# Kernel tuning notes

Hardware: AMD Instinct MI355X
Metric: run time of the kernel (lower is better)

Reference implementation:

```python
import jax, jax.numpy as jnp
import numpy as np

B, C, L, R, UNITS = 256, 32, 64, 64, 128


def setup_inputs() -> dict:
    key = jax.random.key(0)
    ks = jax.random.split(key, 6)
    D = C + 3 * UNITS  # input_dim = channels + 3*units

    def glorot(k, fan_in, fan_out):
        lim = float(np.sqrt(6.0 / (fan_in + fan_out)))
        return jax.random.uniform(k, (fan_in, fan_out), jnp.float32, -lim, lim)

    inputs = jax.random.normal(ks[0], (B, C, L, R), jnp.float32)
    wr = glorot(ks[1], D, 3 * UNITS)
    br = jnp.zeros((3 * UNITS,), jnp.float32)
    wz = glorot(ks[2], D, 4 * UNITS)
    bz = jnp.zeros((4 * UNITS,), jnp.float32)
    # orthogonal init approximated by scaled normal (math of forward unaffected)
    w_ij = jax.random.normal(ks[3], (C, UNITS), jnp.float32) / np.sqrt(C).astype(np.float32)
    b_ij = jnp.zeros((UNITS,), jnp.float32)
    U = jax.random.normal(ks[4], (3 * UNITS, UNITS), jnp.float32) / np.sqrt(3 * UNITS).astype(np.float32)
    return dict(inputs=inputs, wr=wr, br=br, wz=wz, bz=bz, w_ij=w_ij, b_ij=b_ij, U=U)


def _spatial_gru(inputs, wr, br, wz, bz, w_ij, b_ij, U):
    units = b_ij.shape[0]
    x = jnp.transpose(inputs, (2, 3, 0, 1))  # [L, R, B, C]  (direction 'lt')
    Ldim, Rdim, Bdim, _ = x.shape
    zeros = jnp.zeros((Bdim, units), x.dtype)

    def col_step(h_left, cell):
        h_top, h_diag, s_ij = cell  # each [B, units] / [B, C]
        # q = [h_top, h_left, h_diag, s_ij]  (matches torch cat order)
        q = jnp.concatenate([h_top, h_left, h_diag, s_ij], axis=1)
        r = jax.nn.sigmoid(q @ wr + br)                      # [B, 3U]
        z = (q @ wz + bz).reshape(Bdim, 4, units)
        zi, zl, zt, zd = jnp.moveaxis(jax.nn.softmax(z, axis=1), 1, 0)
        h_hat = jnp.tanh(
            s_ij @ w_ij + b_ij
            + (r * jnp.concatenate([h_left, h_top, h_diag], axis=1)) @ U
        )
        h = zl * h_left + zt * h_top + zd * h_diag + zi * h_hat
        return h, h

    def row_step(prev_row, x_row):
        # prev_row[j] is h_top for column j; prev_row[j-1] is h_diag (zero at j=0)
        diag_row = jnp.concatenate([zeros[None], prev_row[:-1]], axis=0)
        _, new_row = jax.lax.scan(col_step, zeros, (prev_row, diag_row, x_row))
        return new_row, None

    init_row = jnp.zeros((Rdim, Bdim, units), x.dtype)
    final_row, _ = jax.lax.scan(row_step, init_row, x)
    return final_row[-1]  # h at bottom-right cell, [B, units]


def reference(inputs, wr, br, wz, bz, w_ij, b_ij, U):
    return _spatial_gru(inputs, wr, br, wz, bz, w_ij, b_ij, U)
```

## Files before the change

### kernel.cpp

```cpp
#include <hip/hip_runtime.h>
#include <cstddef>

typedef _Float16 f16;
typedef unsigned int u32;
typedef __attribute__((ext_vector_type(8))) _Float16 half8;
typedef __attribute__((ext_vector_type(4))) _Float16 half4;
typedef __attribute__((ext_vector_type(4))) float f32x4;

#define BATCH 256
#define CH    32
#define LR    64
#define UNITS 128
#define DIN   416
#define NC    1024
#define KU    384

#define OFF_WH   0ull
#define OFF_WL   745472ull
#define OFF_W3H  1490944ull
#define OFF_W3L  1499136ull
#define OFF_BC   1507328ull
#define OFF_UH   1511424ull
#define OFF_UL   1609728ull
#define OFF_HHI  1708032ull
#define HPLANE   4194304ull
#define OFF_HLO  (OFF_HHI + 3ull*HPLANE)
#define OFF_G    (OFF_HLO + 3ull*HPLANE)

static __device__ __forceinline__ void gll16(const void* g, void* l) {
  __builtin_amdgcn_global_load_lds(
      (const __attribute__((address_space(1))) u32*)g,
      (__attribute__((address_space(3))) u32*)l, 16, 0, 0);
}
static __device__ __forceinline__ float fast_tanh(float x) {
  float e = __expf(-2.f * fabsf(x));
  float t = (1.f - e) / (1.f + e);
  return copysignf(t, x);
}

__global__ __launch_bounds__(256) void prep_kernel(
    const float* __restrict__ wr, const float* __restrict__ br,
    const float* __restrict__ wz, const float* __restrict__ bz,
    const float* __restrict__ w_ij, const float* __restrict__ b_ij,
    const float* __restrict__ U, char* __restrict__ ws) {
  int idx = blockIdx.x * 256 + threadIdx.x;
  if (idx < 896 * DIN) {
    int n = idx / DIN, k = idx % DIN;
    float v = (n < 384) ? wr[k * 384 + n] : wz[k * 512 + (n - 384)];
    f16 hi = (f16)v;
    ((f16*)(ws + OFF_WH))[idx] = hi;
    ((f16*)(ws + OFF_WL))[idx] = (f16)(v - (float)hi);
  }
  if (idx < 128 * 32) {
    int n3 = idx >> 5, k3 = idx & 31;
    float v = w_ij[k3 * UNITS + n3];
    f16 hi = (f16)v;
    ((f16*)(ws + OFF_W3H))[idx] = hi;
    ((f16*)(ws + OFF_W3L))[idx] = (f16)(v - (float)hi);
  }
  if (idx < UNITS * KU) {
    int n = idx / KU, k = idx % KU;
    float v = U[k * UNITS + n];
    f16 hi = (f16)v;
    ((f16*)(ws + OFF_UH))[idx] = hi;
    ((f16*)(ws + OFF_UL))[idx] = (f16)(v - (float)hi);
  }
  if (idx < NC) {
    float b;
    if (idx < 384)      b = br[idx];
    else if (idx < 896) b = bz[idx - 384];
    else                b = b_ij[idx - 896];
    ((float*)(ws + OFF_BC))[idx] = b;
  }
}

__global__ __launch_bounds__(256) void gemm_kernel(
    const float* __restrict__ inputs, char* __restrict__ ws, int d, int i0) {
  const int bx = blockIdx.x;
  const int cb = bx & 7, rb = (bx >> 3) & 1, ci = bx >> 4;
  const int i = i0 + ci, j = d - i;
  const int b0 = rb * 128, n0 = cb * 128;
  const int t = threadIdx.x;
  const int w = t >> 6, lane = t & 63;
  const int lm = lane & 15, ksl = lane >> 4;
  const int wrow = (w >> 1) * 64, wcol = (w & 1) * 64;

  __shared__ f16 Ah[4096], Al[4096], Bh[4096], Bl[4096];

  const int s0 = w * 128 + lane, s1 = s0 + 64;
  const int r0s = s0 >> 2, k0s = (s0 & 3) ^ ((r0s >> 1) & 3);
  const int r1s = s1 >> 2, k1s = (s1 & 3) ^ ((r1s >> 1) & 3);
  const u32 db0 = (u32)w * 2048u, db1 = db0 + 1024u;
  const int kswz = (ksl ^ ((lm >> 1) & 3)) * 8;

  const f16* __restrict__ H1h = (const f16*)(ws + OFF_HHI + (size_t)((d + 2) % 3) * HPLANE);
  const f16* __restrict__ H1l = (const f16*)(ws + OFF_HLO + (size_t)((d + 2) % 3) * HPLANE);
  const f16* __restrict__ H2h = (const f16*)(ws + OFF_HHI + (size_t)((d + 1) % 3) * HPLANE);
  const f16* __restrict__ H2l = (const f16*)(ws + OFF_HLO + (size_t)((d + 1) % 3) * HPLANE);
  const f16* __restrict__ Wh  = (const f16*)(ws + OFF_WH);
  const f16* __restrict__ Wl  = (const f16*)(ws + OFF_WL);
  const f16* __restrict__ W3h = (const f16*)(ws + OFF_W3H);
  const f16* __restrict__ W3l = (const f16*)(ws + OFF_W3L);
  const bool vt = (i > 0), vl = (j > 0), vd = (i > 0 && j > 0);

  f32x4 acc[4][4];
#pragma unroll
  for (int mi = 0; mi < 4; mi++)
#pragma unroll
    for (int ni = 0; ni < 4; ni++)
#pragma unroll
      for (int r = 0; r < 4; r++) acc[mi][ni][r] = 0.f;

  for (int kt = (cb == 7 ? 12 : 0); kt < 13; kt++) {
    const bool ok = (kt < 4) ? vt : (kt < 8) ? vl : (kt < 12) ? vd : true;
    if (!ok) continue;

    if (kt < 12) {
      const f16 *ph, *pl; int hrow;
      if (kt < 4)      { ph = H1h; pl = H1l; hrow = i - 1; }
      else if (kt < 8) { ph = H1h; pl = H1l; hrow = i; }
      else             { ph = H2h; pl = H2l; hrow = i - 1; }
      const size_t ab = ((size_t)hrow * BATCH + b0) * UNITS + (size_t)(kt & 3) * 32;
      gll16(ph + ab + r0s * UNITS + k0s * 8, (char*)Ah + db0);
      gll16(ph + ab + r1s * UNITS + k1s * 8, (char*)Ah + db1);
      gll16(pl + ab + r0s * UNITS + k0s * 8, (char*)Al + db0);
      gll16(pl + ab + r1s * UNITS + k1s * 8, (char*)Al + db1);
    } else {
      const int r = t >> 1, kp = (t & 1) * 2;
      const int b = b0 + r, sw = (r >> 1) & 3;
#pragma unroll
      for (int c2 = 0; c2 < 2; c2++) {
        const int c = kp + c2;
        half8 hv, lv;
#pragma unroll
        for (int q = 0; q < 8; q++) {
          float v = inputs[((size_t)b * CH + c * 8 + q) * (LR * LR) + i * LR + j];
          f16 h = (f16)v;
          hv[q] = h; lv[q] = (f16)(v - (float)h);
        }
        const int p = r * 4 + (c ^ sw);
        *(half8*)&Ah[p * 8] = hv;
        *(half8*)&Al[p * 8] = lv;
      }
    }
    if (cb < 7) {
      const size_t bb = (size_t)n0 * DIN + (size_t)kt * 32;
      gll16(Wh + bb + r0s * DIN + k0s * 8, (char*)Bh + db0);
      gll16(Wh + bb + r1s * DIN + k1s * 8, (char*)Bh + db1);
      gll16(Wl + bb + r0s * DIN + k0s * 8, (char*)Bl + db0);
      gll16(Wl + bb + r1s * DIN + k1s * 8, (char*)Bl + db1);
    } else {
      gll16(W3h + r0s * 32 + k0s * 8, (char*)Bh + db0);
      gll16(W3h + r1s * 32 + k1s * 8, (char*)Bh + db1);
      gll16(W3l + r0s * 32 + k0s * 8, (char*)Bl + db0);
      gll16(W3l + r1s * 32 + k1s * 8, (char*)Bl + db1);
    }
    __syncthreads();

    half8 afh[4], afl[4], bfh[4], bfl[4];
#pragma unroll
    for (int mi = 0; mi < 4; mi++) {
      const int ro = (wrow + mi * 16 + lm) * 32 + kswz;
      afh[mi] = *(const half8*)&Ah[ro];
      afl[mi] = *(const half8*)&Al[ro];
    }
#pragma unroll
    for (int ni = 0; ni < 4; ni++) {
      const int ro = (wcol + ni * 16 + lm) * 32 + kswz;
      bfh[ni] = *(const half8*)&Bh[ro];
      bfl[ni] = *(const half8*)&Bl[ro];
    }
#pragma unroll
    for (int mi = 0; mi < 4; mi++)
#pragma unroll
      for (int ni = 0; ni < 4; ni++) {
        acc[mi][ni] = __builtin_amdgcn_mfma_f32_16x16x32_f16(afh[mi], bfh[ni], acc[mi][ni], 0, 0, 0);
        acc[mi][ni] = __builtin_amdgcn_mfma_f32_16x16x32_f16(afl[mi], bfh[ni], acc[mi][ni], 0, 0, 0);
        acc[mi][ni] = __builtin_amdgcn_mfma_f32_16x16x32_f16(afh[mi], bfl[ni], acc[mi][ni], 0, 0, 0);
      }
    __syncthreads();
  }

  float* __restrict__ G = (float*)(ws + OFF_G) + (size_t)ci * BATCH * NC;
  const float* __restrict__ bc = (const float*)(ws + OFF_BC);
#pragma unroll
  for (int mi = 0; mi < 4; mi++)
#pragma unroll
    for (int ni = 0; ni < 4; ni++) {
      const int n = n0 + wcol + ni * 16 + lm;
      const float bb = bc[n];
#pragma unroll
      for (int r = 0; r < 4; r++) {
        const int b = b0 + wrow + mi * 16 + ksl * 4 + r;
        G[(size_t)b * NC + n] = acc[mi][ni][r] + bb;
      }
    }
}

__global__ __launch_bounds__(256) void gate_kernel(char* __restrict__ ws, int d, int i0) {
  const int bx = blockIdx.x;
  const int rb = bx & 7, ci = bx >> 3;
  const int i = i0 + ci, j = d - i;
  const int b0 = rb * 32;
  const int t = threadIdx.x;
  const int w = t >> 6, lane = t & 63;
  const int lm = lane & 15, ksl = lane >> 4;
  const int wcol = w * 32;

  __shared__ f16 Rh[32][40], Rl[32][40];
  __shared__ f16 Uh[4096], Ul[4096];

  const int s0 = w * 128 + lane, s1 = s0 + 64;
  const int r0s = s0 >> 2, k0s = (s0 & 3) ^ ((r0s >> 1) & 3);
  const int r1s = s1 >> 2, k1s = (s1 & 3) ^ ((r1s >> 1) & 3);
  const u32 db0 = (u32)w * 2048u, db1 = db0 + 1024u;
  const int kswz = (ksl ^ ((lm >> 1) & 3)) * 8;

  float* __restrict__ G = (float*)(ws + OFF_G) + (size_t)ci * BATCH * NC;
  const f16* __restrict__ H1h = (const f16*)(ws + OFF_HHI + (size_t)((d + 2) % 3) * HPLANE);
  const f16* __restrict__ H1l = (const f16*)(ws + OFF_HLO + (size_t)((d + 2) % 3) * HPLANE);
  const f16* __restrict__ H2h = (const f16*)(ws + OFF_HHI + (size_t)((d + 1) % 3) * HPLANE);
  const f16* __restrict__ H2l = (const f16*)(ws + OFF_HLO + (size_t)((d + 1) % 3) * HPLANE);
  f16* __restrict__ Hoh = (f16*)(ws + OFF_HHI + (size_t)(d % 3) * HPLANE);
  f16* __restrict__ Hol = (f16*)(ws + OFF_HLO + (size_t)(d % 3) * HPLANE);
  const f16* __restrict__ UhT = (const f16*)(ws + OFF_UH);
  const f16* __restrict__ UlT = (const f16*)(ws + OFF_UL);
  const bool vt = (i > 0), vlf = (j > 0), vd = (i > 0 && j > 0);

  f32x4 acc[2][2];
#pragma unroll
  for (int mi = 0; mi < 2; mi++)
#pragma unroll
    for (int ni = 0; ni < 2; ni++)
#pragma unroll
      for (int r = 0; r < 4; r++) acc[mi][ni][r] = 0.f;

  const int sr = t >> 3, sk = (t & 7) * 4;

  for (int kt = 0; kt < 12; kt++) {
    const f16 *ph, *pl; int hrow; bool ok;
    if (kt < 4)      { ph = H1h; pl = H1l; hrow = i;     ok = vlf; }
    else if (kt < 8) { ph = H1h; pl = H1l; hrow = i - 1; ok = vt; }
    else             { ph = H2h; pl = H2l; hrow = i - 1; ok = vd; }
    if (!ok) continue;
    {
      const int b = b0 + sr;
      const f32x4 g = *(const f32x4*)&G[(size_t)b * NC + kt * 32 + sk];
      const size_t hx = ((size_t)hrow * BATCH + b) * UNITS + (kt & 3) * 32 + sk;
      const half4 h4 = *(const half4*)(ph + hx);
      const half4 l4 = *(const half4*)(pl + hx);
      half4 oh, ol;
#pragma unroll
      for (int q = 0; q < 4; q++) {
        const float rv = 1.f / (1.f + __expf(-g[q]));
        const float v = rv * ((float)h4[q] + (float)l4[q]);
        const f16 h = (f16)v;
        oh[q] = h; ol[q] = (f16)(v - (float)h);
      }
      *(half4*)&Rh[sr][sk] = oh;
      *(half4*)&Rl[sr][sk] = ol;
    }
    {
      const size_t ub = (size_t)kt * 32;
      gll16(UhT + ub + r0s * KU + k0s * 8, (char*)Uh + db0);
      gll16(UhT + ub + r1s * KU + k1s * 8, (char*)Uh + db1);
      gll16(UlT + ub + r0s * KU + k0s * 8, (char*)Ul + db0);
      gll16(UlT + ub + r1s * KU + k1s * 8, (char*)Ul + db1);
    }
    __syncthreads();

    half8 afh[2], afl[2], bfh[2], bfl[2];
#pragma unroll
    for (int mi = 0; mi < 2; mi++) {
      afh[mi] = *(const half8*)&Rh[mi * 16 + lm][ksl * 8];
      afl[mi] = *(const half8*)&Rl[mi * 16 + lm][ksl * 8];
    }
#pragma unroll
    for (int ni = 0; ni < 2; ni++) {
      const int ro = (wcol + ni * 16 + lm) * 32 + kswz;
      bfh[ni] = *(const half8*)&Uh[ro];
      bfl[ni] = *(const half8*)&Ul[ro];
    }
#pragma unroll
    for (int mi = 0; mi < 2; mi++)
#pragma unroll
      for (int ni = 0; ni < 2; ni++) {
        acc[mi][ni] = __builtin_amdgcn_mfma_f32_16x16x32_f16(afh[mi], bfh[ni], acc[mi][ni], 0, 0, 0);
        acc[mi][ni] = __builtin_amdgcn_mfma_f32_16x16x32_f16(afl[mi], bfh[ni], acc[mi][ni], 0, 0, 0);
        acc[mi][ni] = __builtin_amdgcn_mfma_f32_16x16x32_f16(afh[mi], bfl[ni], acc[mi][ni], 0, 0, 0);
      }
    __syncthreads();
  }

#pragma unroll
  for (int mi = 0; mi < 2; mi++)
#pragma unroll
    for (int r = 0; r < 4; r++) {
      const int b = b0 + mi * 16 + ksl * 4 + r;
      const float* __restrict__ Gr = G + (size_t)b * NC;
      const size_t ho  = ((size_t)i * BATCH + b) * UNITS;
      const size_t htb = ((size_t)(i - 1) * BATCH + b) * UNITS;
#pragma unroll
      for (int ni = 0; ni < 2; ni++) {
        const int u = wcol + ni * 16 + lm;
        const float zi = Gr[384 + u], zl = Gr[512 + u], zt = Gr[640 + u], zd = Gr[768 + u];
        const float mm = fmaxf(fmaxf(zi, zl), fmaxf(zt, zd));
        const float ei = __expf(zi - mm), el = __expf(zl - mm),
                    et = __expf(zt - mm), ed = __expf(zd - mm);
        const float inv = 1.f / (ei + el + et + ed);
        const float hl = vlf ? (float)H1h[ho + u] + (float)H1l[ho + u] : 0.f;
        const float ht = vt  ? (float)H1h[htb + u] + (float)H1l[htb + u] : 0.f;
        const float hd = vd  ? (float)H2h[htb + u] + (float)H2l[htb + u] : 0.f;
        const float hh = fast_tanh(Gr[896 + u] + acc[mi][ni][r]);
        const float h = (el * hl + et * ht + ed * hd + ei * hh) * inv;
        const f16 hhi = (f16)h;
        Hoh[ho + u] = hhi;
        Hol[ho + u] = (f16)(h - (float)hhi);
      }
    }
}

__global__ __launch_bounds__(256) void copy_kernel(const char* __restrict__ ws,
                                                   float* __restrict__ out) {
  int idx = blockIdx.x * 256 + threadIdx.x;
  const f16* Hh = (const f16*)(ws + OFF_HHI);
  const f16* Hl = (const f16*)(ws + OFF_HLO);
  const size_t o = (size_t)63 * BATCH * UNITS + idx;
  out[idx] = (float)Hh[o] + (float)Hl[o];
}

extern "C" void kernel_launch(void* const* d_in, const int* in_sizes, int n_in,
                              void* d_out, int out_size, void* d_ws, size_t ws_size,
                              hipStream_t stream) {
  const float* inputs = (const float*)d_in[0];
  const float* wr     = (const float*)d_in[1];
  const float* br     = (const float*)d_in[2];
  const float* wz     = (const float*)d_in[3];
  const float* bz     = (const float*)d_in[4];
  const float* w_ij   = (const float*)d_in[5];
  const float* b_ij   = (const float*)d_in[6];
  const float* Umat   = (const float*)d_in[7];
  char* ws = (char*)d_ws;

  prep_kernel<<<dim3(1456), dim3(256), 0, stream>>>(
      wr, br, wz, bz, w_ij, b_ij, Umat, ws);

  for (int d = 0; d < 127; d++) {
    int i0 = d > 63 ? d - 63 : 0;
    int i1 = d < 63 ? d : 63;
    int nc = i1 - i0 + 1;
    gemm_kernel<<<dim3(nc * 16), dim3(256), 0, stream>>>(inputs, ws, d, i0);
    gate_kernel<<<dim3(nc * 8), dim3(256), 0, stream>>>(ws, d, i0);
  }

  copy_kernel<<<dim3(128), dim3(256), 0, stream>>>(ws, (float*)d_out);
}
```

Baseline: 12.73 ms.

## Fuse all wavefront diagonals into one persistent cooperative kernel with grid syncs

Merges the prep kernel, the per-diagonal GEMM and gate kernels, and the final copy into one persistent cooperative kernel. Blocks stride over tiles, and grid.sync() stands in for the boundary between each of the 254 kernel launches. This removes per-launch overhead and gaps between the many small dependent launches. In exchange it pays for grid-wide barriers, and occupancy is limited to the co-resident block count (launch bounds now request 2 blocks per CU).

```diff
diff --git a/kernel.cpp b/kernel.cpp
--- a/kernel.cpp
+++ b/kernel.cpp
@@ -1,5 +1,8 @@
 #include <hip/hip_runtime.h>
+#include <hip/hip_cooperative_groups.h>
 #include <cstddef>
+
+namespace cg = cooperative_groups;
 
 typedef _Float16 f16;
 typedef unsigned int u32;
@@ -38,54 +41,19 @@
   return copysignf(t, x);
 }
 
-__global__ __launch_bounds__(256) void prep_kernel(
+__global__ __launch_bounds__(256, 2) void fused_kernel(
+    const float* __restrict__ inputs,
     const float* __restrict__ wr, const float* __restrict__ br,
     const float* __restrict__ wz, const float* __restrict__ bz,
     const float* __restrict__ w_ij, const float* __restrict__ b_ij,
-    const float* __restrict__ U, char* __restrict__ ws) {
-  int idx = blockIdx.x * 256 + threadIdx.x;
-  if (idx < 896 * DIN) {
-    int n = idx / DIN, k = idx % DIN;
-    float v = (n < 384) ? wr[k * 384 + n] : wz[k * 512 + (n - 384)];
-    f16 hi = (f16)v;
-    ((f16*)(ws + OFF_WH))[idx] = hi;
-    ((f16*)(ws + OFF_WL))[idx] = (f16)(v - (float)hi);
-  }
-  if (idx < 128 * 32) {
-    int n3 = idx >> 5, k3 = idx & 31;
-    float v = w_ij[k3 * UNITS + n3];
-    f16 hi = (f16)v;
-    ((f16*)(ws + OFF_W3H))[idx] = hi;
-    ((f16*)(ws + OFF_W3L))[idx] = (f16)(v - (float)hi);
-  }
-  if (idx < UNITS * KU) {
-    int n = idx / KU, k = idx % KU;
-    float v = U[k * UNITS + n];
-    f16 hi = (f16)v;
-    ((f16*)(ws + OFF_UH))[idx] = hi;
-    ((f16*)(ws + OFF_UL))[idx] = (f16)(v - (float)hi);
-  }
-  if (idx < NC) {
-    float b;
-    if (idx < 384)      b = br[idx];
-    else if (idx < 896) b = bz[idx - 384];
-    else                b = b_ij[idx - 896];
-    ((float*)(ws + OFF_BC))[idx] = b;
-  }
-}
-
-__global__ __launch_bounds__(256) void gemm_kernel(
-    const float* __restrict__ inputs, char* __restrict__ ws, int d, int i0) {
-  const int bx = blockIdx.x;
-  const int cb = bx & 7, rb = (bx >> 3) & 1, ci = bx >> 4;
-  const int i = i0 + ci, j = d - i;
-  const int b0 = rb * 128, n0 = cb * 128;
-  const int t = threadIdx.x;
+    const float* __restrict__ Umat, char* __restrict__ ws,
+    float* __restrict__ out) {
+  cg::grid_group grid = cg::this_grid();
+  const int bid = blockIdx.x, nblk = gridDim.x, t = threadIdx.x;
   const int w = t >> 6, lane = t & 63;
   const int lm = lane & 15, ksl = lane >> 4;
-  const int wrow = (w >> 1) * 64, wcol = (w & 1) * 64;
-
-  __shared__ f16 Ah[4096], Al[4096], Bh[4096], Bl[4096];
+
+  __shared__ f16 smA[4096], smB[4096], smC[4096], smD[4096];
 
   const int s0 = w * 128 + lane, s1 = s0 + 64;
   const int r0s = s0 >> 2, k0s = (s0 & 3) ^ ((r0s >> 1) & 3);
@@ -93,240 +61,273 @@
   const u32 db0 = (u32)w * 2048u, db1 = db0 + 1024u;
   const int kswz = (ksl ^ ((lm >> 1) & 3)) * 8;
 
-  const f16* __restrict__ H1h = (const f16*)(ws + OFF_HHI + (size_t)((d + 2) % 3) * HPLANE);
-  const f16* __restrict__ H1l = (const f16*)(ws + OFF_HLO + (size_t)((d + 2) % 3) * HPLANE);
-  const f16* __restrict__ H2h = (const f16*)(ws + OFF_HHI + (size_t)((d + 1) % 3) * HPLANE);
-  const f16* __restrict__ H2l = (const f16*)(ws + OFF_HLO + (size_t)((d + 1) % 3) * HPLANE);
+  for (int idx = bid * 256 + t; idx < 896 * DIN; idx += nblk * 256) {
+    {
+      int n = idx / DIN, k = idx % DIN;
+      float v = (n < 384) ? wr[k * 384 + n] : wz[k * 512 + (n - 384)];
+      f16 hi = (f16)v;
+      ((f16*)(ws + OFF_WH))[idx] = hi;
+      ((f16*)(ws + OFF_WL))[idx] = (f16)(v - (float)hi);
+    }
+    if (idx < 128 * 32) {
+      int n3 = idx >> 5, k3 = idx & 31;
+      float v = w_ij[k3 * UNITS + n3];
+      f16 hi = (f16)v;
+      ((f16*)(ws + OFF_W3H))[idx] = hi;
+      ((f16*)(ws + OFF_W3L))[idx] = (f16)(v - (float)hi);
+    }
+    if (idx < UNITS * KU) {
+      int n = idx / KU, k = idx % KU;
+      float v = Umat[k * UNITS + n];
+      f16 hi = (f16)v;
+      ((f16*)(ws + OFF_UH))[idx] = hi;
+      ((f16*)(ws + OFF_UL))[idx] = (f16)(v - (float)hi);
+    }
+    if (idx < NC) {
+      float b;
+      if (idx < 384)      b = br[idx];
+      else if (idx < 896) b = bz[idx - 384];
+      else                b = b_ij[idx - 896];
+      ((float*)(ws + OFF_BC))[idx] = b;
+    }
+  }
+  grid.sync();
+
   const f16* __restrict__ Wh  = (const f16*)(ws + OFF_WH);
   const f16* __restrict__ Wl  = (const f16*)(ws + OFF_WL);
   const f16* __restrict__ W3h = (const f16*)(ws + OFF_W3H);
   const f16* __restrict__ W3l = (const f16*)(ws + OFF_W3L);
-  const bool vt = (i > 0), vl = (j > 0), vd = (i > 0 && j > 0);
-
-  f32x4 acc[4][4];
-#pragma unroll
-  for (int mi = 0; mi < 4; mi++)
-#pragma unroll
-    for (int ni = 0; ni < 4; ni++)
-#pragma unroll
-      for (int r = 0; r < 4; r++) acc[mi][ni][r] = 0.f;
-
-  for (int kt = (cb == 7 ? 12 : 0); kt < 13; kt++) {
-    const bool ok = (kt < 4) ? vt : (kt < 8) ? vl : (kt < 12) ? vd : true;
-    if (!ok) continue;
-
-    if (kt < 12) {
-      const f16 *ph, *pl; int hrow;
-      if (kt < 4)      { ph = H1h; pl = H1l; hrow = i - 1; }
-      else if (kt < 8) { ph = H1h; pl = H1l; hrow = i; }
-      else             { ph = H2h; pl = H2l; hrow = i - 1; }
-      const size_t ab = ((size_t)hrow * BATCH + b0) * UNITS + (size_t)(kt & 3) * 32;
-      gll16(ph + ab + r0s * UNITS + k0s * 8, (char*)Ah + db0);
-      gll16(ph + ab + r1s * UNITS + k1s * 8, (char*)Ah + db1);
-      gll16(pl + ab + r0s * UNITS + k0s * 8, (char*)Al + db0);
-      gll16(pl + ab + r1s * UNITS + k1s * 8, (char*)Al + db1);
-    } else {
-      const int r = t >> 1, kp = (t & 1) * 2;
-      const int b = b0 + r, sw = (r >> 1) & 3;
-#pragma unroll
-      for (int c2 = 0; c2 < 2; c2++) {
-        const int c = kp + c2;
-        half8 hv, lv;
-#pragma unroll
-        for (int q = 0; q < 8; q++) {
-          float v = inputs[((size_t)b * CH + c * 8 + q) * (LR * LR) + i * LR + j];
-          f16 h = (f16)v;
-          hv[q] = h; lv[q] = (f16)(v - (float)h);
-        }
-        const int p = r * 4 + (c ^ sw);
-        *(half8*)&Ah[p * 8] = hv;
-        *(half8*)&Al[p * 8] = lv;
-      }
-    }
-    if (cb < 7) {
-      const size_t bb = (size_t)n0 * DIN + (size_t)kt * 32;
-      gll16(Wh + bb + r0s * DIN + k0s * 8, (char*)Bh + db0);
-      gll16(Wh + bb + r1s * DIN + k1s * 8, (char*)Bh + db1);
-      gll16(Wl + bb + r0s * DIN + k0s * 8, (char*)Bl + db0);
-      gll16(Wl + bb + r1s * DIN + k1s * 8, (char*)Bl + db1);
-    } else {
-      gll16(W3h + r0s * 32 + k0s * 8, (char*)Bh + db0);
-      gll16(W3h + r1s * 32 + k1s * 8, (char*)Bh + db1);
-      gll16(W3l + r0s * 32 + k0s * 8, (char*)Bl + db0);
-      gll16(W3l + r1s * 32 + k1s * 8, (char*)Bl + db1);
-    }
-    __syncthreads();
-
-    half8 afh[4], afl[4], bfh[4], bfl[4];
-#pragma unroll
-    for (int mi = 0; mi < 4; mi++) {
-      const int ro = (wrow + mi * 16 + lm) * 32 + kswz;
-      afh[mi] = *(const half8*)&Ah[ro];
-      afl[mi] = *(const half8*)&Al[ro];
-    }
-#pragma unroll
-    for (int ni = 0; ni < 4; ni++) {
-      const int ro = (wcol + ni * 16 + lm) * 32 + kswz;
-      bfh[ni] = *(const half8*)&Bh[ro];
-      bfl[ni] = *(const half8*)&Bl[ro];
-    }
-#pragma unroll
-    for (int mi = 0; mi < 4; mi++)
-#pragma unroll
-      for (int ni = 0; ni < 4; ni++) {
-        acc[mi][ni] = __builtin_amdgcn_mfma_f32_16x16x32_f16(afh[mi], bfh[ni], acc[mi][ni], 0, 0, 0);
-        acc[mi][ni] = __builtin_amdgcn_mfma_f32_16x16x32_f16(afl[mi], bfh[ni], acc[mi][ni], 0, 0, 0);
-        acc[mi][ni] = __builtin_amdgcn_mfma_f32_16x16x32_f16(afh[mi], bfl[ni], acc[mi][ni], 0, 0, 0);
-      }
-    __syncthreads();
-  }
-
-  float* __restrict__ G = (float*)(ws + OFF_G) + (size_t)ci * BATCH * NC;
-  const float* __restrict__ bc = (const float*)(ws + OFF_BC);
-#pragma unroll
-  for (int mi = 0; mi < 4; mi++)
-#pragma unroll
-    for (int ni = 0; ni < 4; ni++) {
-      const int n = n0 + wcol + ni * 16 + lm;
-      const float bb = bc[n];
-#pragma unroll
-      for (int r = 0; r < 4; r++) {
-        const int b = b0 + wrow + mi * 16 + ksl * 4 + r;
-        G[(size_t)b * NC + n] = acc[mi][ni][r] + bb;
-      }
-    }
-}
-
-__global__ __launch_bounds__(256) void gate_kernel(char* __restrict__ ws, int d, int i0) {
-  const int bx = blockIdx.x;
-  const int rb = bx & 7, ci = bx >> 3;
-  const int i = i0 + ci, j = d - i;
-  const int b0 = rb * 32;
-  const int t = threadIdx.x;
-  const int w = t >> 6, lane = t & 63;
-  const int lm = lane & 15, ksl = lane >> 4;
-  const int wcol = w * 32;
-
-  __shared__ f16 Rh[32][40], Rl[32][40];
-  __shared__ f16 Uh[4096], Ul[4096];
-
-  const int s0 = w * 128 + lane, s1 = s0 + 64;
-  const int r0s = s0 >> 2, k0s = (s0 & 3) ^ ((r0s >> 1) & 3);
-  const int r1s = s1 >> 2, k1s = (s1 & 3) ^ ((r1s >> 1) & 3);
-  const u32 db0 = (u32)w * 2048u, db1 = db0 + 1024u;
-  const int kswz = (ksl ^ ((lm >> 1) & 3)) * 8;
-
-  float* __restrict__ G = (float*)(ws + OFF_G) + (size_t)ci * BATCH * NC;
-  const f16* __restrict__ H1h = (const f16*)(ws + OFF_HHI + (size_t)((d + 2) % 3) * HPLANE);
-  const f16* __restrict__ H1l = (const f16*)(ws + OFF_HLO + (size_t)((d + 2) % 3) * HPLANE);
-  const f16* __restrict__ H2h = (const f16*)(ws + OFF_HHI + (size_t)((d + 1) % 3) * HPLANE);
-  const f16* __restrict__ H2l = (const f16*)(ws + OFF_HLO + (size_t)((d + 1) % 3) * HPLANE);
-  f16* __restrict__ Hoh = (f16*)(ws + OFF_HHI + (size_t)(d % 3) * HPLANE);
-  f16* __restrict__ Hol = (f16*)(ws + OFF_HLO + (size_t)(d % 3) * HPLANE);
   const f16* __restrict__ UhT = (const f16*)(ws + OFF_UH);
   const f16* __restrict__ UlT = (const f16*)(ws + OFF_UL);
-  const bool vt = (i > 0), vlf = (j > 0), vd = (i > 0 && j > 0);
-
-  f32x4 acc[2][2];
-#pragma unroll
-  for (int mi = 0; mi < 2; mi++)
-#pragma unroll
-    for (int ni = 0; ni < 2; ni++)
-#pragma unroll
-      for (int r = 0; r < 4; r++) acc[mi][ni][r] = 0.f;
-
-  const int sr = t >> 3, sk = (t & 7) * 4;
-
-  for (int kt = 0; kt < 12; kt++) {
-    const f16 *ph, *pl; int hrow; bool ok;
-    if (kt < 4)      { ph = H1h; pl = H1l; hrow = i;     ok = vlf; }
-    else if (kt < 8) { ph = H1h; pl = H1l; hrow = i - 1; ok = vt; }
-    else             { ph = H2h; pl = H2l; hrow = i - 1; ok = vd; }
-    if (!ok) continue;
-    {
-      const int b = b0 + sr;
-      const f32x4 g = *(const f32x4*)&G[(size_t)b * NC + kt * 32 + sk];
-      const size_t hx = ((size_t)hrow * BATCH + b) * UNITS + (kt & 3) * 32 + sk;
-      const half4 h4 = *(const half4*)(ph + hx);
-      const half4 l4 = *(const half4*)(pl + hx);
-      half4 oh, ol;
-#pragma unroll
-      for (int q = 0; q < 4; q++) {
-        const float rv = 1.f / (1.f + __expf(-g[q]));
-        const float v = rv * ((float)h4[q] + (float)l4[q]);
-        const f16 h = (f16)v;
-        oh[q] = h; ol[q] = (f16)(v - (float)h);
+  const float* __restrict__ bc = (const float*)(ws + OFF_BC);
+
+  for (int d = 0; d < 127; d++) {
+    const int i0 = d > 63 ? d - 63 : 0;
+    const int i1d = d < 63 ? d : 63;
+    const int nc = i1d - i0 + 1;
+    const f16* __restrict__ H1h = (const f16*)(ws + OFF_HHI + (size_t)((d + 2) % 3) * HPLANE);
+    const f16* __restrict__ H1l = (const f16*)(ws + OFF_HLO + (size_t)((d + 2) % 3) * HPLANE);
+    const f16* __restrict__ H2h = (const f16*)(ws + OFF_HHI + (size_t)((d + 1) % 3) * HPLANE);
+    const f16* __restrict__ H2l = (const f16*)(ws + OFF_HLO + (size_t)((d + 1) % 3) * HPLANE);
+    f16* __restrict__ Hoh = (f16*)(ws + OFF_HHI + (size_t)(d % 3) * HPLANE);
+    f16* __restrict__ Hol = (f16*)(ws + OFF_HLO + (size_t)(d % 3) * HPLANE);
+
+    for (int tt = bid; tt < nc * 16; tt += nblk) {
+      const int cb = tt & 7, rb = (tt >> 3) & 1, ci = tt >> 4;
+      const int i = i0 + ci, j = d - i;
+      const int b0 = rb * 128, n0 = cb * 128;
+      const int wrow = (w >> 1) * 64, wcol = (w & 1) * 64;
+      const bool vt = (i > 0), vl = (j > 0), vd = (i > 0 && j > 0);
+      f16* const Ah = smA; f16* const Al = smB;
+      f16* const Bh = smC; f16* const Bl = smD;
+
+      f32x4 acc[4][4];
+#pragma unroll
+      for (int mi = 0; mi < 4; mi++)
+#pragma unroll
+        for (int ni = 0; ni < 4; ni++)
+#pragma unroll
+          for (int r = 0; r < 4; r++) acc[mi][ni][r] = 0.f;
+
+      for (int kt = (cb == 7 ? 12 : 0); kt < 13; kt++) {
+        const bool ok = (kt < 4) ? vt : (kt < 8) ? vl : (kt < 12) ? vd : true;
+        if (!ok) continue;
+
+        if (kt < 12) {
+          const f16 *ph, *pl; int hrow;
+          if (kt < 4)      { ph = H1h; pl = H1l; hrow = i - 1; }
+          else if (kt < 8) { ph = H1h; pl = H1l; hrow = i; }
+          else             { ph = H2h; pl = H2l; hrow = i - 1; }
+          const size_t ab = ((size_t)hrow * BATCH + b0) * UNITS + (size_t)(kt & 3) * 32;
+          gll16(ph + ab + r0s * UNITS + k0s * 8, (char*)Ah + db0);
+          gll16(ph + ab + r1s * UNITS + k1s * 8, (char*)Ah + db1);
+          gll16(pl + ab + r0s * UNITS + k0s * 8, (char*)Al + db0);
+          gll16(pl + ab + r1s * UNITS + k1s * 8, (char*)Al + db1);
+        } else {
+          const int r = t >> 1, kp = (t & 1) * 2;
+          const int b = b0 + r, sw = (r >> 1) & 3;
+#pragma unroll
+          for (int c2 = 0; c2 < 2; c2++) {
+            const int c = kp + c2;
+            half8 hv, lv;
+#pragma unroll
+            for (int q = 0; q < 8; q++) {
+              float v = inputs[((size_t)b * CH + c * 8 + q) * (LR * LR) + i * LR + j];
+              f16 h = (f16)v;
+              hv[q] = h; lv[q] = (f16)(v - (float)h);
+            }
+            const int p = r * 4 + (c ^ sw);
+            *(half8*)&Ah[p * 8] = hv;
+            *(half8*)&Al[p * 8] = lv;
+          }
+        }
+        if (cb < 7) {
+          const size_t bb = (size_t)n0 * DIN + (size_t)kt * 32;
+          gll16(Wh + bb + r0s * DIN + k0s * 8, (char*)Bh + db0);
+          gll16(Wh + bb + r1s * DIN + k1s * 8, (char*)Bh + db1);
+          gll16(Wl + bb + r0s * DIN + k0s * 8, (char*)Bl + db0);
+          gll16(Wl + bb + r1s * DIN + k1s * 8, (char*)Bl + db1);
+        } else {
+          gll16(W3h + r0s * 32 + k0s * 8, (char*)Bh + db0);
+          gll16(W3h + r1s * 32 + k1s * 8, (char*)Bh + db1);
+          gll16(W3l + r0s * 32 + k0s * 8, (char*)Bl + db0);
+          gll16(W3l + r1s * 32 + k1s * 8, (char*)Bl + db1);
+        }
+        __syncthreads();
+
+        half8 afh[4], afl[4], bfh[4], bfl[4];
+#pragma unroll
+        for (int mi = 0; mi < 4; mi++) {
+          const int ro = (wrow + mi * 16 + lm) * 32 + kswz;
+          afh[mi] = *(const half8*)&Ah[ro];
+          afl[mi] = *(const half8*)&Al[ro];
+        }
+#pragma unroll
+        for (int ni = 0; ni < 4; ni++) {
+          const int ro = (wcol + ni * 16 + lm) * 32 + kswz;
+          bfh[ni] = *(const half8*)&Bh[ro];
+          bfl[ni] = *(const half8*)&Bl[ro];
+        }
+#pragma unroll
+        for (int mi = 0; mi < 4; mi++)
+#pragma unroll
+          for (int ni = 0; ni < 4; ni++) {
+            acc[mi][ni] = __builtin_amdgcn_mfma_f32_16x16x32_f16(afh[mi], bfh[ni], acc[mi][ni], 0, 0, 0);
+            acc[mi][ni] = __builtin_amdgcn_mfma_f32_16x16x32_f16(afl[mi], bfh[ni], acc[mi][ni], 0, 0, 0);
+            acc[mi][ni] = __builtin_amdgcn_mfma_f32_16x16x32_f16(afh[mi], bfl[ni], acc[mi][ni], 0, 0, 0);
+          }
+        __syncthreads();
       }
-      *(half4*)&Rh[sr][sk] = oh;
-      *(half4*)&Rl[sr][sk] = ol;
-    }
-    {
-      const size_t ub = (size_t)kt * 32;
-      gll16(UhT + ub + r0s * KU + k0s * 8, (char*)Uh + db0);
-      gll16(UhT + ub + r1s * KU + k1s * 8, (char*)Uh + db1);
-      gll16(UlT + ub + r0s * KU + k0s * 8, (char*)Ul + db0);
-      gll16(UlT + ub + r1s * KU + k1s * 8, (char*)Ul + db1);
-    }
-    __syncthreads();
-
-    half8 afh[2], afl[2], bfh[2], bfl[2];
-#pragma unroll
-    for (int mi = 0; mi < 2; mi++) {
-      afh[mi] = *(const half8*)&Rh[mi * 16 + lm][ksl * 8];
-      afl[mi] = *(const half8*)&Rl[mi * 16 + lm][ksl * 8];
-    }
-#pragma unroll
-    for (int ni = 0; ni < 2; ni++) {
-      const int ro = (wcol + ni * 16 + lm) * 32 + kswz;
-      bfh[ni] = *(const half8*)&Uh[ro];
-      bfl[ni] = *(const half8*)&Ul[ro];
-    }
-#pragma unroll
-    for (int mi = 0; mi < 2; mi++)
-#pragma unroll
-      for (int ni = 0; ni < 2; ni++) {
-        acc[mi][ni] = __builtin_amdgcn_mfma_f32_16x16x32_f16(afh[mi], bfh[ni], acc[mi][ni], 0, 0, 0);
-        acc[mi][ni] = __builtin_amdgcn_mfma_f32_16x16x32_f16(afl[mi], bfh[ni], acc[mi][ni], 0, 0, 0);
-        acc[mi][ni] = __builtin_amdgcn_mfma_f32_16x16x32_f16(afh[mi], bfl[ni], acc[mi][ni], 0, 0, 0);
+
+      float* __restrict__ G = (float*)(ws + OFF_G) + (size_t)ci * BATCH * NC;
+#pragma unroll
+      for (int mi = 0; mi < 4; mi++)
+#pragma unroll
+        for (int ni = 0; ni < 4; ni++) {
+          const int n = n0 + wcol + ni * 16 + lm;
+          const float bb = bc[n];
+#pragma unroll
+          for (int r = 0; r < 4; r++) {
+            const int b = b0 + wrow + mi * 16 + ksl * 4 + r;
+            G[(size_t)b * NC + n] = acc[mi][ni][r] + bb;
+          }
+        }
+    }
+    grid.sync();
+
+    for (int tt = bid; tt < nc * 8; tt += nblk) {
+      const int rb = tt & 7, ci = tt >> 3;
+      const int i = i0 + ci, j = d - i;
+      const int b0 = rb * 32;
+      const int wcol = w * 32;
+      const bool vt = (i > 0), vlf = (j > 0), vd = (i > 0 && j > 0);
+      f16 (* const Rh)[40] = (f16(*)[40])smA;
+      f16 (* const Rl)[40] = (f16(*)[40])smB;
+      f16* const Uh = smC; f16* const Ul = smD;
+
+      float* __restrict__ G = (float*)(ws + OFF_G) + (size_t)ci * BATCH * NC;
+
+      f32x4 acc[2][2];
+#pragma unroll
+      for (int mi = 0; mi < 2; mi++)
+#pragma unroll
+        for (int ni = 0; ni < 2; ni++)
+#pragma unroll
+          for (int r = 0; r < 4; r++) acc[mi][ni][r] = 0.f;
+
+      const int sr = t >> 3, sk = (t & 7) * 4;
+
+      for (int kt = 0; kt < 12; kt++) {
+        const f16 *ph, *pl; int hrow; bool ok;
+        if (kt < 4)      { ph = H1h; pl = H1l; hrow = i;     ok = vlf; }
+        else if (kt < 8) { ph = H1h; pl = H1l; hrow = i - 1; ok = vt; }
+        else             { ph = H2h; pl = H2l; hrow = i - 1; ok = vd; }
+        if (!ok) continue;
+        {
+          const int b = b0 + sr;
+          const f32x4 g = *(const f32x4*)&G[(size_t)b * NC + kt * 32 + sk];
+          const size_t hx = ((size_t)hrow * BATCH + b) * UNITS + (kt & 3) * 32 + sk;
+          const half4 h4 = *(const half4*)(ph + hx);
+          const half4 l4 = *(const half4*)(pl + hx);
+          half4 oh, ol;
+#pragma unroll
+          for (int q = 0; q < 4; q++) {
+            const float rv = 1.f / (1.f + __expf(-g[q]));
+            const float v = rv * ((float)h4[q] + (float)l4[q]);
+            const f16 h = (f16)v;
+            oh[q] = h; ol[q] = (f16)(v - (float)h);
+          }
+          *(half4*)&Rh[sr][sk] = oh;
+          *(half4*)&Rl[sr][sk] = ol;
+        }
+        {
+          const size_t ub = (size_t)kt * 32;
+          gll16(UhT + ub + r0s * KU + k0s * 8, (char*)Uh + db0);
+          gll16(UhT + ub + r1s * KU + k1s * 8, (char*)Uh + db1);
+          gll16(UlT + ub + r0s * KU + k0s * 8, (char*)Ul + db0);
+          gll16(UlT + ub + r1s * KU + k1s * 8, (char*)Ul + db1);
+        }
+        __syncthreads();
+
+        half8 afh[2], afl[2], bfh[2], bfl[2];
+#pragma unroll
+        for (int mi = 0; mi < 2; mi++) {
+          afh[mi] = *(const half8*)&Rh[mi * 16 + lm][ksl * 8];
+          afl[mi] = *(const half8*)&Rl[mi * 16 + lm][ksl * 8];
+        }
+#pragma unroll
+        for (int ni = 0; ni < 2; ni++) {
+          const int ro = (wcol + ni * 16 + lm) * 32 + kswz;
+          bfh[ni] = *(const half8*)&Uh[ro];
+          bfl[ni] = *(const half8*)&Ul[ro];
+        }
+#pragma unroll
+        for (int mi = 0; mi < 2; mi++)
+#pragma unroll
+          for (int ni = 0; ni < 2; ni++) {
+            acc[mi][ni] = __builtin_amdgcn_mfma_f32_16x16x32_f16(afh[mi], bfh[ni], acc[mi][ni], 0, 0, 0);
+            acc[mi][ni] = __builtin_amdgcn_mfma_f32_16x16x32_f16(afl[mi], bfh[ni], acc[mi][ni], 0, 0, 0);
+            acc[mi][ni] = __builtin_amdgcn_mfma_f32_16x16x32_f16(afh[mi], bfl[ni], acc[mi][ni], 0, 0, 0);
+          }
+        __syncthreads();
       }
-    __syncthreads();
+
+#pragma unroll
+      for (int mi = 0; mi < 2; mi++)
+#pragma unroll
+        for (int r = 0; r < 4; r++) {
+          const int b = b0 + mi * 16 + ksl * 4 + r;
+          const float* __restrict__ Gr = G + (size_t)b * NC;
+          const size_t ho  = ((size_t)i * BATCH + b) * UNITS;
+          const size_t htb = ((size_t)(i - 1) * BATCH + b) * UNITS;
+#pragma unroll
+          for (int ni = 0; ni < 2; ni++) {
+            const int u = wcol + ni * 16 + lm;
+            const float zi = Gr[384 + u], zl = Gr[512 + u], zt = Gr[640 + u], zd = Gr[768 + u];
+            const float mm = fmaxf(fmaxf(zi, zl), fmaxf(zt, zd));
+            const float ei = __expf(zi - mm), el = __expf(zl - mm),
+                        et = __expf(zt - mm), ed = __expf(zd - mm);
+            const float inv = 1.f / (ei + el + et + ed);
+            const float hl = vlf ? (float)H1h[ho + u] + (float)H1l[ho + u] : 0.f;
+            const float ht = vt  ? (float)H1h[htb + u] + (float)H1l[htb + u] : 0.f;
+            const float hd = vd  ? (float)H2h[htb + u] + (float)H2l[htb + u] : 0.f;
+            const float hh = fast_tanh(Gr[896 + u] + acc[mi][ni][r]);
+            const float h = (el * hl + et * ht + ed * hd + ei * hh) * inv;
+            const f16 hhi = (f16)h;
+            Hoh[ho + u] = hhi;
+            Hol[ho + u] = (f16)(h - (float)hhi);
+          }
+        }
+    }
+    grid.sync();
   }
 
-#pragma unroll
-  for (int mi = 0; mi < 2; mi++)
-#pragma unroll
-    for (int r = 0; r < 4; r++) {
-      const int b = b0 + mi * 16 + ksl * 4 + r;
-      const float* __restrict__ Gr = G + (size_t)b * NC;
-      const size_t ho  = ((size_t)i * BATCH + b) * UNITS;
-      const size_t htb = ((size_t)(i - 1) * BATCH + b) * UNITS;
-#pragma unroll
-      for (int ni = 0; ni < 2; ni++) {
-        const int u = wcol + ni * 16 + lm;
-        const float zi = Gr[384 + u], zl = Gr[512 + u], zt = Gr[640 + u], zd = Gr[768 + u];
-        const float mm = fmaxf(fmaxf(zi, zl), fmaxf(zt, zd));
-        const float ei = __expf(zi - mm), el = __expf(zl - mm),
-                    et = __expf(zt - mm), ed = __expf(zd - mm);
-        const float inv = 1.f / (ei + el + et + ed);
-        const float hl = vlf ? (float)H1h[ho + u] + (float)H1l[ho + u] : 0.f;
-        const float ht = vt  ? (float)H1h[htb + u] + (float)H1l[htb + u] : 0.f;
-        const float hd = vd  ? (float)H2h[htb + u] + (float)H2l[htb + u] : 0.f;
-        const float hh = fast_tanh(Gr[896 + u] + acc[mi][ni][r]);
-        const float h = (el * hl + et * ht + ed * hd + ei * hh) * inv;
-        const f16 hhi = (f16)h;
-        Hoh[ho + u] = hhi;
-        Hol[ho + u] = (f16)(h - (float)hhi);
-      }
-    }
-}
-
-__global__ __launch_bounds__(256) void copy_kernel(const char* __restrict__ ws,
-                                                   float* __restrict__ out) {
-  int idx = blockIdx.x * 256 + threadIdx.x;
-  const f16* Hh = (const f16*)(ws + OFF_HHI);
-  const f16* Hl = (const f16*)(ws + OFF_HLO);
-  const size_t o = (size_t)63 * BATCH * UNITS + idx;
-  out[idx] = (float)Hh[o] + (float)Hl[o];
+  for (int idx = bid * 256 + t; idx < BATCH * UNITS; idx += nblk * 256) {
+    const f16* Hh = (const f16*)(ws + OFF_HHI);
+    const f16* Hl = (const f16*)(ws + OFF_HLO);
+    const size_t o = (size_t)63 * BATCH * UNITS + idx;
+    out[idx] = (float)Hh[o] + (float)Hl[o];
+  }
 }
 
 extern "C" void kernel_launch(void* const* d_in, const int* in_sizes, int n_in,
@@ -340,18 +341,18 @@
   const float* w_ij   = (const float*)d_in[5];
   const float* b_ij   = (const float*)d_in[6];
   const float* Umat   = (const float*)d_in[7];
-  char* ws = (char*)d_ws;
-
-  prep_kernel<<<dim3(1456), dim3(256), 0, stream>>>(
-      wr, br, wz, bz, w_ij, b_ij, Umat, ws);
-
-  for (int d = 0; d < 127; d++) {
-    int i0 = d > 63 ? d - 63 : 0;
-    int i1 = d < 63 ? d : 63;
-    int nc = i1 - i0 + 1;
-    gemm_kernel<<<dim3(nc * 16), dim3(256), 0, stream>>>(inputs, ws, d, i0);
-    gate_kernel<<<dim3(nc * 8), dim3(256), 0, stream>>>(ws, d, i0);
-  }
-
-  copy_kernel<<<dim3(128), dim3(256), 0, stream>>>(ws, (float*)d_out);
+  char* ws  = (char*)d_ws;
+  float* out = (float*)d_out;
+
+  int maxPerCU = 0;
+  if (hipOccupancyMaxActiveBlocksPerMultiprocessor(&maxPerCU, fused_kernel, 256, 0)
+          != hipSuccess || maxPerCU < 1)
+    maxPerCU = 1;
+  if (maxPerCU > 4) maxPerCU = 4;
+  int nblk = maxPerCU * 256;
+
+  void* args[] = {(void*)&inputs, (void*)&wr, (void*)&br, (void*)&wz, (void*)&bz,
+                  (void*)&w_ij, (void*)&b_ij, (void*)&Umat, (void*)&ws, (void*)&out};
+  hipLaunchCooperativeKernel((const void*)fused_kernel, dim3(nblk), dim3(256),
+                             args, 0, stream);
 }
```

Result: slower. 22.37 ms (+75.8%).
